# Optimization experiments

Measured on AMD Instinct MI355X. Metric: run time of the kernel, lower is better.

The kernel has to match this reference:

```python
import jax, jax.numpy as jnp
import numpy as np

N, T, E = 20000, 4, 320000
IN_F, H_F, OUT_F, HEADS = 32, 16, 16, 8
NEG_SLOPE = 0.2


def gat_layer(x, W, al, ar, b, src, dst, n_nodes, heads, f_out):
    # x: [N, T, Fin], W: [Fin, heads*f_out], al/ar: [heads, f_out], b: [heads*f_out]
    feat = (x @ W).reshape(x.shape[0], x.shape[1], heads, f_out)      # [N,T,H,F]
    el = (feat * al).sum(-1)                                          # [N,T,H]
    er = (feat * ar).sum(-1)                                          # [N,T,H]
    e = jax.nn.leaky_relu(el[src] + er[dst], NEG_SLOPE)               # [E,T,H]
    # segment softmax over incoming edges of each destination node
    m = jax.lax.stop_gradient(jax.ops.segment_max(e, dst, num_segments=n_nodes))
    ex = jnp.exp(e - m[dst])
    s = jax.ops.segment_sum(ex, dst, num_segments=n_nodes)
    alpha = ex / s[dst]                                               # [E,T,H]
    msg = feat[src] * alpha[..., None]                                # [E,T,H,F]
    out = jax.ops.segment_sum(msg, dst, num_segments=n_nodes)
    return out + b.reshape(1, 1, heads, f_out)


def setup_inputs() -> dict:
    key = jax.random.key(0)
    ks = jax.random.split(key, 12)
    x = jax.random.normal(ks[0], (N, T, IN_F), dtype=jnp.float32)
    src = jax.random.randint(ks[1], (E,), 0, N)
    dst = jax.random.randint(ks[2], (E,), 0, N)
    s = 0.1
    W1 = jax.random.normal(ks[3], (IN_F, HEADS * H_F), dtype=jnp.float32) * s
    al1 = jax.random.normal(ks[4], (HEADS, H_F), dtype=jnp.float32) * s
    ar1 = jax.random.normal(ks[5], (HEADS, H_F), dtype=jnp.float32) * s
    b1 = jnp.zeros((HEADS * H_F,), dtype=jnp.float32)
    W2 = jax.random.normal(ks[6], (HEADS * H_F, OUT_F), dtype=jnp.float32) * s
    al2 = jax.random.normal(ks[7], (1, OUT_F), dtype=jnp.float32) * s
    ar2 = jax.random.normal(ks[8], (1, OUT_F), dtype=jnp.float32) * s
    b2 = jnp.zeros((OUT_F,), dtype=jnp.float32)
    return {"x": x, "src": src, "dst": dst, "W1": W1, "al1": al1, "ar1": ar1,
            "b1": b1, "W2": W2, "al2": al2, "ar2": ar2, "b2": b2}


def reference(x, src, dst, W1, al1, ar1, b1, W2, al2, ar2, b2):
    n = x.shape[0]
    h = gat_layer(x, W1, al1, ar1, b1, src, dst, n, HEADS, H_F)   # [N,T,H,F]
    h = h.reshape(n, h.shape[1], -1)                              # [N,T,H*F]
    h = gat_layer(h, W2, al2, ar2, b2, src, dst, n, 1, OUT_F)     # [N,T,1,OUT]
    return h.squeeze(2)                                           # [N,T,OUT]
```

## Files before the change

kernel.cpp:

```cpp
#include <hip/hip_runtime.h>
#include <hip/hip_fp16.h>
#include <math.h>

#define NN 20000
#define TT 4
#define EE 320000
#define NT (NN*TT)
#define H1 8
#define C1 128
#define IN_F 32
#define OUT_F 16
#define CAP 96
#define SCAT_BLOCKS 313
#define XCAST_BLOCKS 1250

typedef _Float16 h8 __attribute__((ext_vector_type(8)));
typedef float f32x4 __attribute__((ext_vector_type(4)));

__device__ __forceinline__ float lrelu_exp(float e) {
  e = (e >= 0.f) ? e : 0.2f * e;
  return __expf(e);
}

__global__ __launch_bounds__(256) void k_front(
    const float* __restrict__ x, const float* __restrict__ W1,
    const float* __restrict__ al1, const float* __restrict__ ar1,
    const float* __restrict__ W2, const float* __restrict__ al2,
    const float* __restrict__ ar2,
    const int4* __restrict__ src4, const int4* __restrict__ dst4,
    int* __restrict__ cnt, int* __restrict__ csr96,
    __half* __restrict__ xh, float* __restrict__ el1, float* __restrict__ er1,
    __half* __restrict__ W1hp, __half* __restrict__ W2pp) {
  __shared__ h8 ELERs[64];
  int b = blockIdx.x;
  int tid = threadIdx.x;
  if (b < SCAT_BLOCKS) {
    int e4 = b * 256 + tid;
    if (e4 < EE / 4) {
      int4 s = src4[e4];
      int4 d = dst4[e4];
      int p0 = atomicAdd(&cnt[d.x], 1); csr96[d.x * CAP + p0] = s.x;
      int p1 = atomicAdd(&cnt[d.y], 1); csr96[d.y * CAP + p1] = s.y;
      int p2 = atomicAdd(&cnt[d.z], 1); csr96[d.z * CAP + p2] = s.z;
      int p3 = atomicAdd(&cnt[d.w], 1); csr96[d.w * CAP + p3] = s.w;
    }
    return;
  }
  if (b == SCAT_BLOCKS) {
    for (int idx = tid; idx < 8 * 512; idx += 256) {
      int tile = idx >> 9;
      int rem = idx & 511;
      int lane = rem >> 3, j = rem & 7;
      int k = (lane >> 4) * 8 + j;
      int n = lane & 15;
      W1hp[idx] = __float2half(W1[k * C1 + tile * 16 + n]);
    }
    for (int idx = tid; idx < 8 * 512; idx += 256) {
      int tile = idx >> 9;
      int rem = idx & 511;
      int lane = rem >> 3, j = rem & 7;
      int ks = tile & 3;
      int k = ks * 32 + (lane >> 4) * 8 + j;
      int n = lane & 15;
      float v = 0.f;
      if (tile < 4) {
        v = W2[k * OUT_F + n];
      } else if (n == 0) {
        float s = 0.f;
        for (int f = 0; f < 16; ++f) s += W2[k * OUT_F + f] * al2[f];
        v = s;
      } else if (n == 1) {
        float s = 0.f;
        for (int f = 0; f < 16; ++f) s += W2[k * OUT_F + f] * ar2[f];
        v = s;
      }
      W2pp[idx] = __float2half(v);
    }
    return;
  }
  {
    __half* E = (__half*)ELERs;
    for (int idx = tid; idx < 512; idx += 256) {
      int lane = idx >> 3, j = idx & 7;
      int k = (lane >> 4) * 8 + j;
      int n = lane & 15;
      int hh_ = n & 7;
      const float* a = (n < 8) ? al1 : ar1;
      float s = 0.f;
      for (int f = 0; f < 16; ++f) s += W1[k * C1 + hh_ * 16 + f] * a[hh_ * 16 + f];
      E[idx] = __float2half(s);
    }
  }
  __syncthreads();
  int wave = tid >> 6, lane = tid & 63;
  int m = lane & 15, quad = lane >> 4;
  int rowbase = (b - SCAT_BLOCKS - 1) * 64 + wave * 16;
  int row = rowbase + m;
  const float4* xp = (const float4*)(x + row * IN_F + quad * 8);
  float4 a0 = xp[0], a1 = xp[1];
  h8 af;
  af[0] = (_Float16)a0.x; af[1] = (_Float16)a0.y;
  af[2] = (_Float16)a0.z; af[3] = (_Float16)a0.w;
  af[4] = (_Float16)a1.x; af[5] = (_Float16)a1.y;
  af[6] = (_Float16)a1.z; af[7] = (_Float16)a1.w;
  *(h8*)(xh + (size_t)row * IN_F + quad * 8) = af;
  {
    h8 bf = ELERs[lane];
    f32x4 c = {0.f, 0.f, 0.f, 0.f};
    c = __builtin_amdgcn_mfma_f32_16x16x32_f16(af, bf, c, 0, 0, 0);
#pragma unroll
    for (int r = 0; r < 4; ++r) {
      int orow = rowbase + quad * 4 + r;
      if (m < 8) el1[orow * H1 + m] = c[r];
      else       er1[orow * H1 + (m - 8)] = c[r];
    }
  }
}

__global__ __launch_bounds__(256) void k_agg1x(
    const __half* __restrict__ xh,
    const float* __restrict__ el1,
    const float* __restrict__ er1,
    const int* __restrict__ cnt, const int* __restrict__ csr96,
    __half* __restrict__ aggx) {
  int tid = threadIdx.x;
  int wv = tid >> 6, lane = tid & 63;
  int n = blockIdx.x * 4 + wv;
  int slot = lane >> 1;
  int t = lane >> 4;
  int hf = lane & 1;
  float er_i = er1[(size_t)n * 32 + slot];
  int deg = cnt[n];
  const int* eb = csr96 + (size_t)n * CAP;
  h8 accA = {0, 0, 0, 0, 0, 0, 0, 0};
  h8 accB = {0, 0, 0, 0, 0, 0, 0, 0};
  float l = 0.f;
  for (int chunk = 0; chunk < deg; chunk += 64) {
    int m = min(64, deg - chunk);
    int sv = (lane < m) ? eb[chunk + lane] : 0;
    int iters = (m + 3) >> 2;
    for (int g = 0; g < iters; ++g) {
      int j = g * 4;
      int s0 = __builtin_amdgcn_readlane(sv, j + 0);
      int s1 = __builtin_amdgcn_readlane(sv, j + 1);
      int s2 = __builtin_amdgcn_readlane(sv, j + 2);
      int s3 = __builtin_amdgcn_readlane(sv, j + 3);
      float ew0 = el1[(size_t)s0 * 32 + slot];
      float ew1 = el1[(size_t)s1 * 32 + slot];
      float ew2 = el1[(size_t)s2 * 32 + slot];
      float ew3 = el1[(size_t)s3 * 32 + slot];
      const __half* x0 = xh + (size_t)(s0 * 4 + t) * 32 + hf * 16;
      const __half* x1 = xh + (size_t)(s1 * 4 + t) * 32 + hf * 16;
      const __half* x2 = xh + (size_t)(s2 * 4 + t) * 32 + hf * 16;
      const __half* x3 = xh + (size_t)(s3 * 4 + t) * 32 + hf * 16;
      h8 a0 = *(const h8*)x0, b0 = *(const h8*)(x0 + 8);
      h8 a1 = *(const h8*)x1, b1_ = *(const h8*)(x1 + 8);
      h8 a2 = *(const h8*)x2, b2_ = *(const h8*)(x2 + 8);
      h8 a3 = *(const h8*)x3, b3_ = *(const h8*)(x3 + 8);
#define CONSUME(K, EW, XA, XB)                                    \
      {                                                           \
        float w_ = lrelu_exp(EW + er_i);                          \
        w_ = (j + K < m) ? w_ : 0.f;                              \
        l += w_;                                                  \
        _Float16 wh_ = (_Float16)w_;                              \
        h8 w8_ = {wh_, wh_, wh_, wh_, wh_, wh_, wh_, wh_};        \
        accA += w8_ * XA;                                         \
        accB += w8_ * XB;                                         \
      }
      CONSUME(0, ew0, a0, b0) CONSUME(1, ew1, a1, b1_)
      CONSUME(2, ew2, a2, b2_) CONSUME(3, ew3, a3, b3_)
#undef CONSUME
    }
  }
  float inv = (l > 0.f) ? (1.f / l) : 0.f;
  h8 r0, r1;
#pragma unroll
  for (int q = 0; q < 8; ++q) {
    r0[q] = (_Float16)((float)accA[q] * inv);
    r1[q] = (_Float16)((float)accB[q] * inv);
  }
  int hh_ = slot & 7;
  __half* op = aggx + (size_t)(n * 4 + t) * 256 + hh_ * 32 + hf * 16;
  *(h8*)op = r0;
  *(h8*)(op + 8) = r1;
}

__global__ __launch_bounds__(256) void k_mid2(
    const __half* __restrict__ aggx,
    const __half* __restrict__ W1hp, const float* __restrict__ b1,
    const __half* __restrict__ W2pp,
    __half* __restrict__ feat2h, float* __restrict__ el2, float* __restrict__ er2) {
  __shared__ __half hs[4][16][C1];
  int tid = threadIdx.x;
  int wave = tid >> 6, lane = tid & 63;
  int m = lane & 15, quad = lane >> 4;
  int rowbase = blockIdx.x * 64 + wave * 16;
  const h8* bp1 = (const h8*)W1hp;
#pragma unroll
  for (int hh_ = 0; hh_ < 8; ++hh_) {
    h8 af = *(const h8*)(aggx + (size_t)(rowbase + m) * 256 + hh_ * 32 + quad * 8);
    f32x4 c = {0.f, 0.f, 0.f, 0.f};
    c = __builtin_amdgcn_mfma_f32_16x16x32_f16(af, bp1[hh_ * 64 + lane], c, 0, 0, 0);
    float bv = b1[hh_ * 16 + m];
#pragma unroll
    for (int r = 0; r < 4; ++r)
      hs[wave][quad * 4 + r][hh_ * 16 + m] = __float2half(c[r] + bv);
  }
  const h8* bp2 = (const h8*)W2pp;
  f32x4 cF = {0.f, 0.f, 0.f, 0.f};
  f32x4 cE = {0.f, 0.f, 0.f, 0.f};
#pragma unroll
  for (int ks = 0; ks < 4; ++ks) {
    h8 af = *(const h8*)&hs[wave][m][ks * 32 + quad * 8];
    cF = __builtin_amdgcn_mfma_f32_16x16x32_f16(af, bp2[ks * 64 + lane], cF, 0, 0, 0);
    cE = __builtin_amdgcn_mfma_f32_16x16x32_f16(af, bp2[(4 + ks) * 64 + lane], cE, 0, 0, 0);
  }
#pragma unroll
  for (int r = 0; r < 4; ++r) {
    int orow = rowbase + quad * 4 + r;
    feat2h[(size_t)orow * OUT_F + m] = __float2half(cF[r]);
    if (m == 0) el2[orow] = cE[r];
    if (m == 1) er2[orow] = cE[r];
  }
}

__global__ __launch_bounds__(256) void k_agg2x(
    const __half* __restrict__ feat2h,
    const float* __restrict__ el2, const float* __restrict__ er2,
    const int* __restrict__ cnt, const int* __restrict__ csr96,
    const float* __restrict__ b2, float* __restrict__ out) {
  int tid = threadIdx.x;
  int wv = tid >> 6, lane = tid & 63;
  int n = blockIdx.x * 4 + wv;
  int t = lane >> 4, f = lane & 15;
  float ern = er2[n * 4 + t];
  int deg = cnt[n];
  const int* eb = csr96 + (size_t)n * CAP;
  float acc = 0.f, l = 0.f;
  for (int chunk = 0; chunk < deg; chunk += 64) {
    int m = min(64, deg - chunk);
    int sv = (lane < m) ? eb[chunk + lane] : 0;
    int iters = (m + 7) >> 3;
    for (int g = 0; g < iters; ++g) {
      int j = g * 8;
      int s0 = __builtin_amdgcn_readlane(sv, j + 0);
      int s1 = __builtin_amdgcn_readlane(sv, j + 1);
      int s2 = __builtin_amdgcn_readlane(sv, j + 2);
      int s3 = __builtin_amdgcn_readlane(sv, j + 3);
      int s4 = __builtin_amdgcn_readlane(sv, j + 4);
      int s5 = __builtin_amdgcn_readlane(sv, j + 5);
      int s6 = __builtin_amdgcn_readlane(sv, j + 6);
      int s7 = __builtin_amdgcn_readlane(sv, j + 7);
      float e0 = el2[s0 * 4 + t];
      float e1 = el2[s1 * 4 + t];
      float e2 = el2[s2 * 4 + t];
      float e3 = el2[s3 * 4 + t];
      float e4 = el2[s4 * 4 + t];
      float e5 = el2[s5 * 4 + t];
      float e6 = el2[s6 * 4 + t];
      float e7 = el2[s7 * 4 + t];
      __half f0 = feat2h[(size_t)(s0 * 4 + t) * OUT_F + f];
      __half f1 = feat2h[(size_t)(s1 * 4 + t) * OUT_F + f];
      __half f2 = feat2h[(size_t)(s2 * 4 + t) * OUT_F + f];
      __half f3 = feat2h[(size_t)(s3 * 4 + t) * OUT_F + f];
      __half f4 = feat2h[(size_t)(s4 * 4 + t) * OUT_F + f];
      __half f5 = feat2h[(size_t)(s5 * 4 + t) * OUT_F + f];
      __half f6 = feat2h[(size_t)(s6 * 4 + t) * OUT_F + f];
      __half f7 = feat2h[(size_t)(s7 * 4 + t) * OUT_F + f];
#define CONSUME(K, EW, FV)                                        \
      {                                                           \
        float w_ = lrelu_exp(EW + ern);                           \
        w_ = (j + K < m) ? w_ : 0.f;                              \
        l += w_;                                                  \
        acc = fmaf(w_, __half2float(FV), acc);                    \
      }
      CONSUME(0, e0, f0) CONSUME(1, e1, f1)
      CONSUME(2, e2, f2) CONSUME(3, e3, f3)
      CONSUME(4, e4, f4) CONSUME(5, e5, f5)
      CONSUME(6, e6, f6) CONSUME(7, e7, f7)
#undef CONSUME
    }
  }
  float inv = (l > 0.f) ? (1.f / l) : 0.f;
  out[(size_t)(n * 4 + t) * OUT_F + f] = acc * inv + b2[f];
}

extern "C" void kernel_launch(void* const* d_in, const int* in_sizes, int n_in,
                              void* d_out, int out_size, void* d_ws, size_t ws_size,
                              hipStream_t stream) {
  const float* x   = (const float*)d_in[0];
  const int*   src = (const int*)d_in[1];
  const int*   dst = (const int*)d_in[2];
  const float* W1  = (const float*)d_in[3];
  const float* al1 = (const float*)d_in[4];
  const float* ar1 = (const float*)d_in[5];
  const float* b1  = (const float*)d_in[6];
  const float* W2  = (const float*)d_in[7];
  const float* al2 = (const float*)d_in[8];
  const float* ar2 = (const float*)d_in[9];
  const float* b2  = (const float*)d_in[10];
  float* out = (float*)d_out;

  char* w = (char*)d_ws;
  __half* xh     = (__half*)w; w += (size_t)NT * IN_F * 2;
  __half* aggx   = (__half*)w; w += (size_t)NT * 256 * 2;
  __half* feat2h = (__half*)w; w += (size_t)NT * OUT_F * 2;
  float*  el1    = (float*)w;  w += (size_t)NT * H1 * 4;
  float*  er1    = (float*)w;  w += (size_t)NT * H1 * 4;
  float*  el2    = (float*)w;  w += (size_t)NT * 4;
  float*  er2    = (float*)w;  w += (size_t)NT * 4;
  __half* W1hp   = (__half*)w; w += (size_t)8 * 512 * 2;
  __half* W2pp   = (__half*)w; w += (size_t)8 * 512 * 2;
  int* cnt     = (int*)w;      w += (size_t)NN * 4;
  int* csr96   = (int*)w;      w += (size_t)NN * CAP * 4;

  hipMemsetAsync(cnt, 0, NN * sizeof(int), stream);

  k_front<<<SCAT_BLOCKS + 1 + XCAST_BLOCKS, 256, 0, stream>>>(
      x, W1, al1, ar1, W2, al2, ar2, (const int4*)src, (const int4*)dst,
      cnt, csr96, xh, el1, er1, W1hp, W2pp);
  k_agg1x<<<NN / 4, 256, 0, stream>>>(xh, el1, er1, cnt, csr96, aggx);
  k_mid2<<<NT / 64, 256, 0, stream>>>(aggx, W1hp, b1, W2pp, feat2h, el2, er2);
  k_agg2x<<<NN / 4, 256, 0, stream>>>(feat2h, el2, er2, cnt, csr96, b2, out);
}
```

Before: 157.5 us.

## Fuse layer-1 aggregation with mid-stage MFMA projections via shared memory

Merges the layer-1 neighbour aggregation kernel with the following kernel that applies W1, the bias and the W2/attention projections. Aggregated features now stay in LDS instead of going through a global fp16 buffer of NT*256 halves, which removes one launch and that write/read round trip. Each block handles 16 rows: its four waves split the eight heads for the first MFMA, then only wave 0 runs the second projection. The costs are two block barriers, more LDS per block, and three idle waves during the final stage.

Result: faster. 151.4 us (median of 2 runs) (-3.9%).

```diff
diff --git a/kernel.cpp b/kernel.cpp
--- a/kernel.cpp
+++ b/kernel.cpp
@@ -117,12 +117,17 @@
   }
 }
 
-__global__ __launch_bounds__(256) void k_agg1x(
+__global__ __launch_bounds__(256) void k_agg1m(
     const __half* __restrict__ xh,
     const float* __restrict__ el1,
     const float* __restrict__ er1,
     const int* __restrict__ cnt, const int* __restrict__ csr96,
-    __half* __restrict__ aggx) {
+    const __half* __restrict__ W1hp, const float* __restrict__ b1,
+    const __half* __restrict__ W2pp,
+    __half* __restrict__ feat2h, float* __restrict__ el2,
+    float* __restrict__ er2) {
+  __shared__ __half axs[16][264];
+  __shared__ __half hs[16][136];
   int tid = threadIdx.x;
   int wv = tid >> 6, lane = tid & 63;
   int n = blockIdx.x * 4 + wv;
@@ -173,51 +178,47 @@
     }
   }
   float inv = (l > 0.f) ? (1.f / l) : 0.f;
-  h8 r0, r1;
-#pragma unroll
-  for (int q = 0; q < 8; ++q) {
-    r0[q] = (_Float16)((float)accA[q] * inv);
-    r1[q] = (_Float16)((float)accB[q] * inv);
-  }
-  int hh_ = slot & 7;
-  __half* op = aggx + (size_t)(n * 4 + t) * 256 + hh_ * 32 + hf * 16;
-  *(h8*)op = r0;
-  *(h8*)(op + 8) = r1;
-}
-
-__global__ __launch_bounds__(256) void k_mid2(
-    const __half* __restrict__ aggx,
-    const __half* __restrict__ W1hp, const float* __restrict__ b1,
-    const __half* __restrict__ W2pp,
-    __half* __restrict__ feat2h, float* __restrict__ el2, float* __restrict__ er2) {
-  __shared__ __half hs[4][16][C1];
-  int tid = threadIdx.x;
-  int wave = tid >> 6, lane = tid & 63;
+  {
+    h8 r0, r1;
+#pragma unroll
+    for (int q = 0; q < 8; ++q) {
+      r0[q] = (_Float16)((float)accA[q] * inv);
+      r1[q] = (_Float16)((float)accB[q] * inv);
+    }
+    int hh_ = slot & 7;
+    __half* op = &axs[wv * 4 + t][hh_ * 32 + hf * 16];
+    *(h8*)op = r0;
+    *(h8*)(op + 8) = r1;
+  }
+  __syncthreads();
+
   int m = lane & 15, quad = lane >> 4;
-  int rowbase = blockIdx.x * 64 + wave * 16;
   const h8* bp1 = (const h8*)W1hp;
 #pragma unroll
-  for (int hh_ = 0; hh_ < 8; ++hh_) {
-    h8 af = *(const h8*)(aggx + (size_t)(rowbase + m) * 256 + hh_ * 32 + quad * 8);
+  for (int hi = 0; hi < 2; ++hi) {
+    int head = wv * 2 + hi;
+    h8 af = *(const h8*)&axs[m][head * 32 + quad * 8];
     f32x4 c = {0.f, 0.f, 0.f, 0.f};
-    c = __builtin_amdgcn_mfma_f32_16x16x32_f16(af, bp1[hh_ * 64 + lane], c, 0, 0, 0);
-    float bv = b1[hh_ * 16 + m];
+    c = __builtin_amdgcn_mfma_f32_16x16x32_f16(af, bp1[head * 64 + lane], c, 0, 0, 0);
+    float bv = b1[head * 16 + m];
 #pragma unroll
     for (int r = 0; r < 4; ++r)
-      hs[wave][quad * 4 + r][hh_ * 16 + m] = __float2half(c[r] + bv);
-  }
+      hs[quad * 4 + r][head * 16 + m] = __float2half(c[r] + bv);
+  }
+  __syncthreads();
+  if (wv != 0) return;
   const h8* bp2 = (const h8*)W2pp;
   f32x4 cF = {0.f, 0.f, 0.f, 0.f};
   f32x4 cE = {0.f, 0.f, 0.f, 0.f};
 #pragma unroll
   for (int ks = 0; ks < 4; ++ks) {
-    h8 af = *(const h8*)&hs[wave][m][ks * 32 + quad * 8];
+    h8 af = *(const h8*)&hs[m][ks * 32 + quad * 8];
     cF = __builtin_amdgcn_mfma_f32_16x16x32_f16(af, bp2[ks * 64 + lane], cF, 0, 0, 0);
     cE = __builtin_amdgcn_mfma_f32_16x16x32_f16(af, bp2[(4 + ks) * 64 + lane], cE, 0, 0, 0);
   }
 #pragma unroll
   for (int r = 0; r < 4; ++r) {
-    int orow = rowbase + quad * 4 + r;
+    int orow = blockIdx.x * 16 + quad * 4 + r;
     feat2h[(size_t)orow * OUT_F + m] = __float2half(cF[r]);
     if (m == 0) el2[orow] = cE[r];
     if (m == 1) er2[orow] = cE[r];
@@ -303,7 +304,6 @@
 
   char* w = (char*)d_ws;
   __half* xh     = (__half*)w; w += (size_t)NT * IN_F * 2;
-  __half* aggx   = (__half*)w; w += (size_t)NT * 256 * 2;
   __half* feat2h = (__half*)w; w += (size_t)NT * OUT_F * 2;
   float*  el1    = (float*)w;  w += (size_t)NT * H1 * 4;
   float*  er1    = (float*)w;  w += (size_t)NT * H1 * 4;
@@ -319,7 +319,7 @@
   k_front<<<SCAT_BLOCKS + 1 + XCAST_BLOCKS, 256, 0, stream>>>(
       x, W1, al1, ar1, W2, al2, ar2, (const int4*)src, (const int4*)dst,
       cnt, csr96, xh, el1, er1, W1hp, W2pp);
-  k_agg1x<<<NN / 4, 256, 0, stream>>>(xh, el1, er1, cnt, csr96, aggx);
-  k_mid2<<<NT / 64, 256, 0, stream>>>(aggx, W1hp, b1, W2pp, feat2h, el2, er2);
+  k_agg1m<<<NN / 4, 256, 0, stream>>>(xh, el1, er1, cnt, csr96,
+                                      W1hp, b1, W2pp, feat2h, el2, er2);
   k_agg2x<<<NN / 4, 256, 0, stream>>>(feat2h, el2, er2, cnt, csr96, b2, out);
 }
```
